# Performance work log

Hardware: AMD Instinct MI355X
Metric: run time of the kernel (lower is better)

The kernel has to match this reference:

```python
import jax, jax.numpy as jnp
import numpy as np

N = 100000      # nodes
F_IN = 500      # num_features
H = 128         # num_hidden
C = 40          # num_classes
E = 3200000     # structural edges
K = 5           # knn neighbors


def setup_inputs() -> dict:
    key = jax.random.key(0)
    ks = jax.random.split(key, 9)
    x = jax.random.normal(ks[0], (N, F_IN), dtype=jnp.float32)
    edge_index = jax.random.randint(ks[1], (2, E), 0, N, dtype=jnp.int64)
    # knn graph: source i repeated K times, targets random (stand-in for cosine-KNN)
    src = jnp.repeat(jnp.arange(N, dtype=jnp.int64), K)
    dst = jax.random.randint(ks[2], (K * N,), 0, N, dtype=jnp.int64)
    edge_index_knn = jnp.stack([src, dst])
    s = lambda f: np.float32(1.0 / np.sqrt(f))
    W1 = jax.random.normal(ks[3], (F_IN, H), jnp.float32) * s(F_IN)
    b1 = jnp.zeros((H,), jnp.float32)
    W2 = jax.random.normal(ks[4], (2 * H, C), jnp.float32) * s(2 * H)
    b2 = jnp.zeros((C,), jnp.float32)
    Wlin = jax.random.normal(ks[5], (C, 2 * C), jnp.float32) * s(2 * C)  # torch Linear layout [out,in]
    blin = jnp.zeros((C,), jnp.float32)
    return {"x": x, "edge_index": edge_index, "edge_index_knn": edge_index_knn,
            "W1": W1, "b1": b1, "W2": W2, "b2": b2, "Wlin": Wlin, "blin": blin}


def gcn_conv(x, W, b, edge_index):
    # PyG GCNConv: add self-loops, symmetric normalization deg^-1/2 A deg^-1/2, x@W, scatter-add, +bias
    n = x.shape[0]
    loop = jnp.arange(n, dtype=edge_index.dtype)
    row = jnp.concatenate([edge_index[0], loop])  # sources (gathered)
    col = jnp.concatenate([edge_index[1], loop])  # targets (scattered)
    deg = jax.ops.segment_sum(jnp.ones_like(col, x.dtype), col, num_segments=n)
    dinv = jnp.where(deg > 0, jax.lax.rsqrt(jnp.maximum(deg, 1e-12)), 0.0).astype(x.dtype)
    norm = dinv[row] * dinv[col]                      # [E+n]
    h = x @ W                                          # [n, out]
    agg = jax.ops.segment_sum(h[row] * norm[:, None], col, num_segments=n)
    return agg + b


def reference(x, edge_index, edge_index_knn, W1, b1, W2, b2, Wlin, blin):
    h1 = gcn_conv(x, W1, b1, edge_index)
    h1_2 = gcn_conv(x, W1, b1, edge_index_knn)
    R1 = jax.nn.relu(jnp.concatenate([h1, h1_2], axis=1))  # dropout identity (eval mode)
    h2 = gcn_conv(R1, W2, b2, edge_index)
    h2_2 = gcn_conv(R1, W2, b2, edge_index_knn)
    R2 = jnp.concatenate([h2, h2_2], axis=1)
    logits = R2 @ Wlin.T + blin
    return jax.nn.log_softmax(logits, axis=1)
```

## Files before the change

kernel.cpp:

```cpp
#include <hip/hip_runtime.h>
#include <stdint.h>

#define NN   100000
#define FIN  500
#define HID  128
#define KP1  512
#define K2   256
#define CO   40
#define NPQ  80
#define NPQP 128
#define NBUCK 391
#define CAPB_S 9216
#define CAPB_K 1536

typedef __attribute__((ext_vector_type(8))) short short8;
typedef __attribute__((ext_vector_type(4))) float float4v;
typedef __attribute__((address_space(3))) unsigned int as3_u32;
typedef __attribute__((address_space(1))) unsigned int as1_u32;

__device__ __forceinline__ unsigned short f2bf(float f) {
  unsigned u = __float_as_uint(f);
  u = u + 0x7fffu + ((u >> 16) & 1u);
  return (unsigned short)(u >> 16);
}
__device__ __forceinline__ float bf2f(unsigned short s) {
  return __uint_as_float(((unsigned)s) << 16);
}
__device__ __forceinline__ void gl_lds16(const void* g, void* l) {
  __builtin_amdgcn_global_load_lds((const as1_u32*)g, (as3_u32*)l, 16, 0, 0);
}

__global__ __launch_bounds__(256) void k_bin(
    const int* __restrict__ ei, int nS, int nb1S, int* __restrict__ gcur_s, int* __restrict__ gbin_s,
    const int* __restrict__ eik, int nK, int* __restrict__ gcur_k, int* __restrict__ gbin_k) {
  __shared__ int cnt[NBUCK];
  __shared__ int base[NBUCK];
  const int b = blockIdx.x;
  const bool knn = (b >= nb1S);
  const int* src = knn ? eik      : ei;
  const int* tgt = knn ? eik + nK : ei + nS;
  const int n    = knn ? nK : nS;
  int* gcur      = knn ? gcur_k : gcur_s;
  int* gbin      = knn ? gbin_k : gbin_s;
  const int capb = knn ? CAPB_K : CAPB_S;
  const int ebase = (knn ? b - nb1S : b) * 4096;
  const int t = threadIdx.x;

  for (int i = t; i < NBUCK; i += 256) cnt[i] = 0;
  __syncthreads();
  int s[16], g[16];
#pragma unroll
  for (int i = 0; i < 16; ++i) {
    const int e = ebase + i * 256 + t;
    const bool v = e < n;
    s[i] = v ? src[e] : 0;
    g[i] = v ? tgt[e] : -1;
    if (v) atomicAdd(&cnt[g[i] >> 8], 1);
  }
  __syncthreads();
  for (int i = t; i < NBUCK; i += 256) {
    const int c = cnt[i];
    base[i] = c ? atomicAdd(&gcur[i], c) : 0;
    cnt[i] = 0;
  }
  __syncthreads();
#pragma unroll
  for (int i = 0; i < 16; ++i) {
    if (g[i] >= 0) {
      const int bkt = g[i] >> 8;
      const int pos = base[bkt] + atomicAdd(&cnt[bkt], 1);
      if (pos < capb) gbin[bkt * capb + pos] = (s[i] << 8) | (g[i] & 255);
    }
  }
}

__global__ __launch_bounds__(512) void k_bscan(const int* __restrict__ gcur_s, int* __restrict__ bscan_s,
                                               const int* __restrict__ gcur_k, int* __restrict__ bscan_k) {
  __shared__ int sd[512];
  const int* gcur = blockIdx.x ? gcur_k : gcur_s;
  int* bscan      = blockIdx.x ? bscan_k : bscan_s;
  const int t = threadIdx.x;
  const int v = (t < NBUCK) ? gcur[t] : 0;
  sd[t] = v;
  __syncthreads();
  for (int off = 1; off < 512; off <<= 1) {
    const int x = (t >= off) ? sd[t - off] : 0;
    __syncthreads(); sd[t] += x; __syncthreads();
  }
  if (t < NBUCK) bscan[t] = sd[t] - v;
}

__global__ __launch_bounds__(256) void k_csr(
    const int* __restrict__ gcur_s, const int* __restrict__ gbin_s, const int* __restrict__ bscan_s,
    int* __restrict__ rp_s, int2* __restrict__ colw_s, float* __restrict__ dinv_s,
    const int* __restrict__ gcur_k, const int* __restrict__ gbin_k, const int* __restrict__ bscan_k,
    int* __restrict__ rp_k, int2* __restrict__ colw_k, float* __restrict__ dinv_k) {
  __shared__ int cnt[256];
  __shared__ int base[256];
  const int b0 = blockIdx.x;
  const bool knn = (b0 >= NBUCK);
  const int b = knn ? b0 - NBUCK : b0;
  const int* gcur  = knn ? gcur_k  : gcur_s;
  const int* gbin  = knn ? gbin_k  : gbin_s;
  const int* bscan = knn ? bscan_k : bscan_s;
  int* rp     = knn ? rp_k   : rp_s;
  int2* colw  = knn ? colw_k : colw_s;
  float* dinv = knn ? dinv_k : dinv_s;
  const int capb = knn ? CAPB_K : CAPB_S;
  const int t = threadIdx.x;
  int nB = gcur[b]; if (nB > capb) nB = capb;
  const int gb0 = b * capb;
  const int gbase = bscan[b];

  cnt[t] = 0;
  __syncthreads();
  for (int i = t; i < nB; i += 256) atomicAdd(&cnt[gbin[gb0 + i] & 255], 1);
  __syncthreads();
  const int myc = cnt[t];
  base[t] = myc;
  __syncthreads();
  for (int off = 1; off < 256; off <<= 1) {
    const int x = (t >= off) ? base[t - off] : 0;
    __syncthreads(); base[t] += x; __syncthreads();
  }
  const int excl = base[t] - myc;
  const int tg = b * 256 + t;
  if (tg < NN) { rp[tg] = gbase + excl; dinv[tg] = rsqrtf((float)(myc + 1)); }
  if (tg == NN) rp[NN] = gbase + excl;
  __syncthreads();
  base[t] = excl; cnt[t] = 0;
  __syncthreads();
  for (int i = t; i < nB; i += 256) {
    const int e = gbin[gb0 + i];
    const int tl = e & 255;
    const int pos = atomicAdd(&cnt[tl], 1);
    colw[gbase + base[tl] + pos] = make_int2(e >> 8, 0);
  }
}

__global__ __launch_bounds__(256) void k_fuse(
    int2* __restrict__ colw_s, const float* __restrict__ dinv_s, int nS, int nbF,
    int2* __restrict__ colw_k, const float* __restrict__ dinv_k, int nK) {
  const int b = blockIdx.x;
  if (b < nbF) {
    const int i = b * 256 + threadIdx.x;
    if (i < nS) {
      const int s = colw_s[i].x;
      colw_s[i].y = __float_as_int(dinv_s[s]);
    }
  } else {
    const int i = (b - nbF) * 256 + threadIdx.x;
    if (i < nK) {
      const int s = colw_k[i].x;
      colw_k[i].y = __float_as_int(dinv_k[s]);
    }
  }
}

__global__ void k_w1t(const float* __restrict__ W1, unsigned short* __restrict__ W1T) {
  int idx = blockIdx.x * 256 + threadIdx.x;
  int n = idx >> 9, k = idx & 511;
  float v = (k < FIN) ? W1[k * HID + n] : 0.f;
  W1T[idx] = f2bf(v);
}
__global__ void k_wpq(const float* __restrict__ W2, const float* __restrict__ Wl,
                      const float* __restrict__ b2, const float* __restrict__ bl,
                      unsigned short* __restrict__ WpqT, float* __restrict__ cb) {
  const int idx = blockIdx.x * 256 + threadIdx.x;
  const int n = idx >> 8, k = idx & 255;
  const int o = (n < CO) ? n : n - CO;
  const int joff = (n < CO) ? 0 : CO;
  float s = 0.f;
#pragma unroll 8
  for (int j = 0; j < CO; ++j) s += W2[k * CO + j] * Wl[o * NPQ + joff + j];
  WpqT[n * K2 + k] = f2bf(s);
  if (blockIdx.x == 0 && threadIdx.x < CO) {
    const int oo = threadIdx.x;
    float c = bl[oo];
    for (int j = 0; j < CO; ++j) c += b2[j] * (Wl[oo * NPQ + j] + Wl[oo * NPQ + CO + j]);
    cb[oo] = c;
  }
}

__global__ __launch_bounds__(256) void k_gemm1(const float* __restrict__ x,
    const unsigned short* __restrict__ W1T, const float* __restrict__ zbuf,
    unsigned short* __restrict__ H1b) {
  __shared__ float Als[2][512 * 4];
  __shared__ unsigned short Bls[2][512 * 8];
  const int t = threadIdx.x;
  const int wv = t >> 6, lane = t & 63;
  const int qd = lane >> 4, mr = lane & 15;
  const int m0 = blockIdx.x * 64;

  float4v acc[8];
  const float4v zf4 = {0.f, 0.f, 0.f, 0.f};
#pragma unroll
  for (int b = 0; b < 8; ++b) acc[b] = zf4;

  auto stage = [&](int kk, int pb) {
    const int k0 = kk * 32;
#pragma unroll
    for (int i = 0; i < 2; ++i) {
      const int q = (wv * 2 + i) * 64 + lane;
      const int m = q >> 3;
      const int kg = (q & 7) ^ (m & 7);
      const int gm = m0 + m, kb = k0 + kg * 4;
      const float* gp = (gm < NN && kb < FIN) ? (x + (size_t)gm * FIN + kb) : zbuf;
      gl_lds16(gp, &Als[pb][q * 4]);
    }
#pragma unroll
    for (int i = 0; i < 2; ++i) {
      const int q = (wv * 2 + i) * 64 + lane;
      const int n = q >> 2;
      const int kg = (q & 3) ^ ((q >> 3) & 3);
      gl_lds16(W1T + n * KP1 + k0 + kg * 8, &Bls[pb][q * 8]);
    }
  };

  stage(0, 0);
  for (int kk = 0; kk < 16; ++kk) {
    const int cur = kk & 1;
    if (kk + 1 < 16) {
      stage(kk + 1, cur ^ 1);
      asm volatile("s_waitcnt vmcnt(4)" ::: "memory");
    } else {
      asm volatile("s_waitcnt vmcnt(0)" ::: "memory");
    }
    __builtin_amdgcn_s_barrier();

    short8 af;
    {
      const int m = wv * 16 + mr;
      const int s0 = m * 8 + ((2 * qd) ^ (m & 7));
      const int s1 = m * 8 + ((2 * qd + 1) ^ (m & 7));
      const float4v a0 = *(const float4v*)&Als[cur][s0 * 4];
      const float4v a1 = *(const float4v*)&Als[cur][s1 * 4];
      af[0] = (short)f2bf(a0[0]); af[1] = (short)f2bf(a0[1]);
      af[2] = (short)f2bf(a0[2]); af[3] = (short)f2bf(a0[3]);
      af[4] = (short)f2bf(a1[0]); af[5] = (short)f2bf(a1[1]);
      af[6] = (short)f2bf(a1[2]); af[7] = (short)f2bf(a1[3]);
    }
#pragma unroll
    for (int ct = 0; ct < 8; ++ct) {
      const int n = ct * 16 + mr;
      const int sb = n * 4 + (qd ^ ((n >> 1) & 3));
      const short8 bf = *(const short8*)&Bls[cur][sb * 8];
      acc[ct] = __builtin_amdgcn_mfma_f32_16x16x32_bf16(af, bf, acc[ct], 0, 0, 0);
    }
    __builtin_amdgcn_s_barrier();
  }

  const int rb = m0 + wv * 16 + qd * 4;
#pragma unroll
  for (int ct = 0; ct < 8; ++ct) {
    const int col = ct * 16 + mr;
#pragma unroll
    for (int j = 0; j < 4; ++j) {
      const int r = rb + j;
      if (r < NN) H1b[(size_t)r * HID + col] = f2bf(acc[ct][j]);
    }
  }
}

__global__ __launch_bounds__(256) void k_gemm2(const unsigned short* __restrict__ R1b,
    const unsigned short* __restrict__ WpqT, const unsigned short* __restrict__ zbuf,
    unsigned short* __restrict__ PQ) {
  __shared__ unsigned short Als[2][256 * 8];
  __shared__ unsigned short Bls[2][512 * 8];
  const int t = threadIdx.x;
  const int wv = t >> 6, lane = t & 63;
  const int qd = lane >> 4, mr = lane & 15;
  const int m0 = blockIdx.x * 64;

  float4v acc[5];
  const float4v zf4 = {0.f, 0.f, 0.f, 0.f};
#pragma unroll
  for (int b = 0; b < 5; ++b) acc[b] = zf4;

  auto stage = [&](int kk, int pb) {
    const int k0 = kk * 32;
    {
      const int q = wv * 64 + lane;
      const int m = q >> 2;
      const int kg = (q & 3) ^ ((q >> 3) & 3);
      const int gm = m0 + m;
      const unsigned short* gp = (gm < NN) ? (R1b + (size_t)gm * K2 + k0 + kg * 8) : zbuf;
      gl_lds16(gp, &Als[pb][q * 8]);
    }
#pragma unroll
    for (int i = 0; i < 2; ++i) {
      const int q = (wv * 2 + i) * 64 + lane;
      const int n = q >> 2;
      const int kg = (q & 3) ^ ((q >> 3) & 3);
      gl_lds16(WpqT + n * K2 + k0 + kg * 8, &Bls[pb][q * 8]);
    }
  };

  stage(0, 0);
  for (int kk = 0; kk < 8; ++kk) {
    const int cur = kk & 1;
    if (kk + 1 < 8) {
      stage(kk + 1, cur ^ 1);
      asm volatile("s_waitcnt vmcnt(3)" ::: "memory");
    } else {
      asm volatile("s_waitcnt vmcnt(0)" ::: "memory");
    }
    __builtin_amdgcn_s_barrier();

    short8 af;
    {
      const int m = wv * 16 + mr;
      const int sa = m * 4 + (qd ^ ((m >> 1) & 3));
      af = *(const short8*)&Als[cur][sa * 8];
    }
#pragma unroll
    for (int ct = 0; ct < 5; ++ct) {
      const int n = ct * 16 + mr;
      const int sb = n * 4 + (qd ^ ((n >> 1) & 3));
      const short8 bf = *(const short8*)&Bls[cur][sb * 8];
      acc[ct] = __builtin_amdgcn_mfma_f32_16x16x32_bf16(af, bf, acc[ct], 0, 0, 0);
    }
    __builtin_amdgcn_s_barrier();
  }

  const int rb = m0 + wv * 16 + qd * 4;
#pragma unroll
  for (int ct = 0; ct < 5; ++ct) {
    const int col = ct * 16 + mr;
#pragma unroll
    for (int j = 0; j < 4; ++j) {
      const int r = rb + j;
      if (r < NN) PQ[(size_t)r * NPQ + col] = f2bf(acc[ct][j]);
    }
  }
}

__device__ __forceinline__ void ld8(const int2* __restrict__ cw, int base, int e1, bool full,
                                    int2* __restrict__ q) {
  if (full) {
#pragma unroll
    for (int j = 0; j < 8; ++j) q[j] = cw[base + j];
  } else {
    const int e1c = e1 - 1;
#pragma unroll
    for (int j = 0; j < 8; ++j) {
      const int ee = base + j;
      int2 t = cw[(ee < e1) ? ee : e1c];
      t.y = (ee < e1) ? t.y : 0;
      q[j] = t;
    }
  }
}
__device__ __forceinline__ void g8(const int2* __restrict__ q,
    const unsigned* __restrict__ H32, int lane, unsigned* __restrict__ d) {
#pragma unroll
  for (int j = 0; j < 8; ++j) d[j] = H32[(size_t)q[j].x * 64 + lane];
}
__device__ __forceinline__ void f8(const int2* __restrict__ q, const unsigned* __restrict__ d,
                                   float& ax, float& ay) {
#pragma unroll
  for (int j = 0; j < 8; ++j) {
    const float w = __int_as_float(q[j].y);
    ax += w * __uint_as_float(d[j] << 16);
    ay += w * __uint_as_float(d[j] & 0xffff0000u);
  }
}

__global__ __launch_bounds__(256) void k_agg1(
    const int* __restrict__ rp_s, const int2* __restrict__ colw_s, const float* __restrict__ dinv_s,
    const int* __restrict__ rp_k, const int2* __restrict__ colw_k, const float* __restrict__ dinv_k,
    const unsigned short* __restrict__ H, const float* __restrict__ bias,
    unsigned short* __restrict__ out) {
  const int wv = threadIdx.x >> 6, lane = threadIdx.x & 63;
  const int c = blockIdx.x * 4 + wv;
  if (c >= NN) return;
  const unsigned* H32 = (const unsigned*)H;
  const int e0s = __builtin_amdgcn_readfirstlane(rp_s[c]);
  const int e1s = __builtin_amdgcn_readfirstlane(rp_s[c + 1]);
  const int e0k = __builtin_amdgcn_readfirstlane(rp_k[c]);
  const int e1k = __builtin_amdgcn_readfirstlane(rp_k[c + 1]);
  const int nbS = (e1s - e0s + 7) >> 3;
  const int nbK = (e1k - e0k + 7) >> 3;

  int2 q0[8], q1[8], qk[8];
  unsigned d0[8], d1[8], dk[8];
  const unsigned pc = H32[(size_t)c * 64 + lane];
  if (nbS > 0) { ld8(colw_s, e0s, e1s, e0s + 8 <= e1s, q0); g8(q0, H32, lane, d0); }
  if (nbS > 1) { ld8(colw_s, e0s + 8, e1s, e0s + 16 <= e1s, q1); g8(q1, H32, lane, d1); }
  if (nbK > 0) { ld8(colw_k, e0k, e1k, e0k + 8 <= e1k, qk); g8(qk, H32, lane, dk); }

  const float dcs = dinv_s[c], dck = dinv_k[c];
  const float slo = __uint_as_float(pc << 16);
  const float shi = __uint_as_float(pc & 0xffff0000u);
  float ax = dcs * slo, ay = dcs * shi;
  float bx = dck * slo, by = dck * shi;

  int b = 0;
  while (b + 2 < nbS) {
    f8(q0, d0, ax, ay);
    {
      const int bs = e0s + (b + 2) * 8;
      ld8(colw_s, bs, e1s, bs + 8 <= e1s, q0);
      g8(q0, H32, lane, d0);
    }
    f8(q1, d1, ax, ay);
    if (b + 3 < nbS) {
      const int bs = e0s + (b + 3) * 8;
      ld8(colw_s, bs, e1s, bs + 8 <= e1s, q1);
      g8(q1, H32, lane, d1);
    }
    b += 2;
  }
  if (b < nbS) f8(q0, d0, ax, ay);
  if (b + 1 < nbS) f8(q1, d1, ax, ay);

  if (nbK > 0) f8(qk, dk, bx, by);
  for (int bk = 1; bk < nbK; ++bk) {
    const int bs = e0k + bk * 8;
    ld8(colw_k, bs, e1k, bs + 8 <= e1k, qk);
    g8(qk, H32, lane, dk);
    f8(qk, dk, bx, by);
  }

  const float2 bb = ((const float2*)bias)[lane];
  const float o0 = fmaxf(dcs * ax + bb.x, 0.f);
  const float o1 = fmaxf(dcs * ay + bb.y, 0.f);
  const float o2 = fmaxf(dck * bx + bb.x, 0.f);
  const float o3 = fmaxf(dck * by + bb.y, 0.f);
  unsigned* orow = (unsigned*)(out + (size_t)c * K2);
  orow[lane]      = (unsigned)f2bf(o0) | ((unsigned)f2bf(o1) << 16);
  orow[64 + lane] = (unsigned)f2bf(o2) | ((unsigned)f2bf(o3) << 16);
}

__global__ __launch_bounds__(256) void k_aggf(
    const int* __restrict__ rp_s, const int2* __restrict__ colw_s, const float* __restrict__ dinv_s,
    const int* __restrict__ rp_k, const int2* __restrict__ colw_k, const float* __restrict__ dinv_k,
    const unsigned short* __restrict__ PQ, const float* __restrict__ cb,
    float* __restrict__ out) {
  const int wv = threadIdx.x >> 6, lane = threadIdx.x & 63;
  const int c = blockIdx.x * 4 + wv;
  if (c >= NN) return;
  const unsigned* PQ32 = (const unsigned*)PQ;
  const int g = lane / 20;
  const int l = lane % 20;
  float sx = 0.f, sy = 0.f, kx = 0.f, ky = 0.f;
  if (g < 3) {
    {
      const int e1 = rp_s[c + 1];
      int e = rp_s[c] + g;
      for (; e + 9 < e1; e += 12) {
        const int2 q0 = colw_s[e], q1 = colw_s[e + 3], q2 = colw_s[e + 6], q3 = colw_s[e + 9];
        const unsigned d0 = PQ32[(size_t)q0.x * 40 + l];
        const unsigned d1 = PQ32[(size_t)q1.x * 40 + l];
        const unsigned d2 = PQ32[(size_t)q2.x * 40 + l];
        const unsigned d3 = PQ32[(size_t)q3.x * 40 + l];
        const float w0 = __int_as_float(q0.y), w1 = __int_as_float(q1.y);
        const float w2 = __int_as_float(q2.y), w3 = __int_as_float(q3.y);
        sx += w0 * __uint_as_float(d0 << 16) + w1 * __uint_as_float(d1 << 16)
            + w2 * __uint_as_float(d2 << 16) + w3 * __uint_as_float(d3 << 16);
        sy += w0 * __uint_as_float(d0 & 0xffff0000u) + w1 * __uint_as_float(d1 & 0xffff0000u)
            + w2 * __uint_as_float(d2 & 0xffff0000u) + w3 * __uint_as_float(d3 & 0xffff0000u);
      }
      for (; e < e1; e += 3) {
        const int2 q = colw_s[e];
        const unsigned d = PQ32[(size_t)q.x * 40 + l];
        const float w = __int_as_float(q.y);
        sx += w * __uint_as_float(d << 16);
        sy += w * __uint_as_float(d & 0xffff0000u);
      }
    }
    {
      const int e1 = rp_k[c + 1];
      int e = rp_k[c] + g;
      for (; e < e1; e += 3) {
        const int2 q = colw_k[e];
        const unsigned d = PQ32[(size_t)q.x * 40 + 20 + l];
        const float w = __int_as_float(q.y);
        kx += w * __uint_as_float(d << 16);
        ky += w * __uint_as_float(d & 0xffff0000u);
      }
    }
  }
  sx += __shfl(sx, lane + 20) + __shfl(sx, lane + 40);
  sy += __shfl(sy, lane + 20) + __shfl(sy, lane + 40);
  kx += __shfl(kx, lane + 20) + __shfl(kx, lane + 40);
  ky += __shfl(ky, lane + 20) + __shfl(ky, lane + 40);

  float lo = 0.f, hi = 0.f;
  if (lane < 20) {
    const float dcs = dinv_s[c], dck = dinv_k[c];
    const unsigned dP = PQ32[(size_t)c * 40 + lane];
    const unsigned dQ = PQ32[(size_t)c * 40 + 20 + lane];
    const float2 cbb = ((const float2*)cb)[lane];
    lo = dcs * (sx + dcs * __uint_as_float(dP << 16))
       + dck * (kx + dck * __uint_as_float(dQ << 16)) + cbb.x;
    hi = dcs * (sy + dcs * __uint_as_float(dP & 0xffff0000u))
       + dck * (ky + dck * __uint_as_float(dQ & 0xffff0000u)) + cbb.y;
  }
  float m = (lane < 20) ? fmaxf(lo, hi) : -3.4e38f;
#pragma unroll
  for (int off = 1; off < 64; off <<= 1) m = fmaxf(m, __shfl_xor(m, off));
  float s = (lane < 20) ? (expf(lo - m) + expf(hi - m)) : 0.f;
#pragma unroll
  for (int off = 1; off < 64; off <<= 1) s += __shfl_xor(s, off);
  const float lse = m + logf(s);
  if (lane < 20) {
    float2 o; o.x = lo - lse; o.y = hi - lse;
    ((float2*)(out + (size_t)c * CO))[lane] = o;
  }
}

extern "C" void kernel_launch(void* const* d_in, const int* in_sizes, int n_in,
                              void* d_out, int out_size, void* d_ws, size_t ws_size,
                              hipStream_t stream) {
  const float* x  = (const float*)d_in[0];
  const int* ei   = (const int*)d_in[1];
  const int* eik  = (const int*)d_in[2];
  const float* W1 = (const float*)d_in[3];
  const float* b1 = (const float*)d_in[4];
  const float* W2 = (const float*)d_in[5];
  const float* b2 = (const float*)d_in[6];
  const float* Wl = (const float*)d_in[7];
  const float* bl = (const float*)d_in[8];
  float* out = (float*)d_out;
  const int E  = in_sizes[1] / 2;
  const int EK = in_sizes[2] / 2;

  char* p = (char*)d_ws;
  size_t off = 0;
  auto alloc = [&](size_t bytes) -> void* {
    void* r = (void*)(p + off);
    off += (bytes + 255) & ~(size_t)255;
    return r;
  };
  int* gcur_s = (int*)alloc((size_t)NBUCK * 4);
  int* gcur_k = (int*)alloc((size_t)NBUCK * 4);
  void* zbuf = alloc(256);
  const size_t zero_span = off;
  int* bscan_s = (int*)alloc((size_t)NBUCK * 4);
  int* bscan_k = (int*)alloc((size_t)NBUCK * 4);
  float* dinv_s = (float*)alloc((size_t)NN * 4);
  float* dinv_k = (float*)alloc((size_t)NN * 4);
  int* rp_s = (int*)alloc((size_t)(NN + 1) * 4);
  int* rp_k = (int*)alloc((size_t)(NN + 1) * 4);
  unsigned short* W1T = (unsigned short*)alloc((size_t)HID * KP1 * 2);
  unsigned short* WpqT = (unsigned short*)alloc((size_t)NPQP * K2 * 2);
  float* cbv = (float*)alloc((size_t)CO * 4);
  int* gbin_s = (int*)alloc((size_t)NBUCK * CAPB_S * 4);
  int* gbin_k = (int*)alloc((size_t)NBUCK * CAPB_K * 4);
  int2* colw_s = (int2*)alloc((size_t)E * 8);
  int2* colw_k = (int2*)alloc((size_t)EK * 8);
  unsigned short* H1b = (unsigned short*)alloc((size_t)NN * HID * 2);
  unsigned short* R1b = (unsigned short*)alloc((size_t)NN * K2 * 2);
  unsigned short* PQ = H1b;

  hipMemsetAsync(d_ws, 0, zero_span, stream);

  const int nb1S = (E + 4095) / 4096;
  const int nb1K = (EK + 4095) / 4096;
  k_bin<<<nb1S + nb1K, 256, 0, stream>>>(ei, E, nb1S, gcur_s, gbin_s, eik, EK, gcur_k, gbin_k);
  k_bscan<<<2, 512, 0, stream>>>(gcur_s, bscan_s, gcur_k, bscan_k);
  k_csr<<<2 * NBUCK, 256, 0, stream>>>(gcur_s, gbin_s, bscan_s, rp_s, colw_s, dinv_s,
                                       gcur_k, gbin_k, bscan_k, rp_k, colw_k, dinv_k);
  const int nbF = (E + 255) / 256;
  const int nbFk = (EK + 255) / 256;
  k_fuse<<<nbF + nbFk, 256, 0, stream>>>(colw_s, dinv_s, E, nbF, colw_k, dinv_k, EK);

  k_w1t<<<(HID * KP1) / 256, 256, 0, stream>>>(W1, W1T);
  k_wpq<<<NPQ, 256, 0, stream>>>(W2, Wl, b2, bl, WpqT, cbv);

  k_gemm1<<<(NN + 63) / 64, 256, 0, stream>>>(x, W1T, (const float*)zbuf, H1b);
  const int nbAgg = (NN + 3) / 4;
  k_agg1<<<nbAgg, 256, 0, stream>>>(rp_s, colw_s, dinv_s, rp_k, colw_k, dinv_k, H1b, b1, R1b);

  k_gemm2<<<(NN + 63) / 64, 256, 0, stream>>>(R1b, WpqT, (const unsigned short*)zbuf, PQ);
  k_aggf<<<nbAgg, 256, 0, stream>>>(rp_s, colw_s, dinv_s, rp_k, colw_k, dinv_k, PQ, cbv, out);
}
```

Measured before the change: 688.8 us.

## Software-pipeline edge-block gathers in final aggregation kernel with double buffering

Rewrites k_aggf so each wave loads 12-edge blocks of CSR entries with wave-uniform bounds taken through readfirstlane. The PQ gathers for the next two structural blocks are issued before the current block is accumulated, so gather latency overlaps with the FMAs. Partial blocks are padded by clamping the index and zeroing the weight, and the self-row PQ loads are hoisted to the start of the kernel. The cost is higher register pressure from three 12-entry buffers, plus redundant gathers on padded and idle lanes.

Measured after the change: 671.8 us. -2.5%, faster.

```diff
diff --git a/kernel.cpp b/kernel.cpp
--- a/kernel.cpp
+++ b/kernel.cpp
@@ -432,6 +432,43 @@
   orow[64 + lane] = (unsigned)f2bf(o2) | ((unsigned)f2bf(o3) << 16);
 }
 
+__device__ __forceinline__ void ld12(const int2* __restrict__ cw, int base, int e1, bool full,
+                                     int2* __restrict__ q) {
+  if (full) {
+#pragma unroll
+    for (int j = 0; j < 12; ++j) q[j] = cw[base + j];
+  } else {
+    const int e1c = e1 - 1;
+#pragma unroll
+    for (int j = 0; j < 12; ++j) {
+      const int ee = base + j;
+      int2 t = cw[(ee < e1) ? ee : e1c];
+      t.y = (ee < e1) ? t.y : 0;
+      q[j] = t;
+    }
+  }
+}
+__device__ __forceinline__ void gt4(const int2* __restrict__ q, const unsigned* __restrict__ PQ32,
+                                    int g, int l, int off, float* __restrict__ w,
+                                    unsigned* __restrict__ d) {
+#pragma unroll
+  for (int t = 0; t < 4; ++t) {
+    const int2 qa = q[3 * t], qb = q[3 * t + 1], qc = q[3 * t + 2];
+    const int xs = (g == 0) ? qa.x : ((g == 1) ? qb.x : qc.x);
+    const int wi = (g == 0) ? qa.y : ((g == 1) ? qb.y : qc.y);
+    w[t] = __int_as_float(wi);
+    d[t] = PQ32[(size_t)xs * 40 + off + l];
+  }
+}
+__device__ __forceinline__ void ct4(const float* __restrict__ w, const unsigned* __restrict__ d,
+                                    float& sx, float& sy) {
+#pragma unroll
+  for (int t = 0; t < 4; ++t) {
+    sx += w[t] * __uint_as_float(d[t] << 16);
+    sy += w[t] * __uint_as_float(d[t] & 0xffff0000u);
+  }
+}
+
 __global__ __launch_bounds__(256) void k_aggf(
     const int* __restrict__ rp_s, const int2* __restrict__ colw_s, const float* __restrict__ dinv_s,
     const int* __restrict__ rp_k, const int2* __restrict__ colw_k, const float* __restrict__ dinv_k,
@@ -441,46 +478,57 @@
   const int c = blockIdx.x * 4 + wv;
   if (c >= NN) return;
   const unsigned* PQ32 = (const unsigned*)PQ;
-  const int g = lane / 20;
-  const int l = lane % 20;
+  const int g = (lane < 60) ? (lane / 20) : 2;
+  const int l = lane - 20 * g;
+
+  const int e0s = __builtin_amdgcn_readfirstlane(rp_s[c]);
+  const int e1s = __builtin_amdgcn_readfirstlane(rp_s[c + 1]);
+  const int e0k = __builtin_amdgcn_readfirstlane(rp_k[c]);
+  const int e1k = __builtin_amdgcn_readfirstlane(rp_k[c + 1]);
+  const int nbS = (e1s - e0s + 11) / 12;
+  const int nbK = (e1k - e0k + 11) / 12;
+
+  unsigned dP = 0, dQ = 0;
+  if (lane < 20) {
+    dP = PQ32[(size_t)c * 40 + lane];
+    dQ = PQ32[(size_t)c * 40 + 20 + lane];
+  }
+
+  int2 q0[12], q1[12], qk[12];
+  float w0[4], w1[4], wk[4];
+  unsigned d0[4], d1[4], dk[4];
+  if (nbS > 0) { ld12(colw_s, e0s, e1s, e0s + 12 <= e1s, q0); gt4(q0, PQ32, g, l, 0, w0, d0); }
+  if (nbS > 1) { ld12(colw_s, e0s + 12, e1s, e0s + 24 <= e1s, q1); gt4(q1, PQ32, g, l, 0, w1, d1); }
+  if (nbK > 0) { ld12(colw_k, e0k, e1k, e0k + 12 <= e1k, qk); gt4(qk, PQ32, g, l, 20, wk, dk); }
+
   float sx = 0.f, sy = 0.f, kx = 0.f, ky = 0.f;
-  if (g < 3) {
+  int b = 0;
+  while (b + 2 < nbS) {
+    ct4(w0, d0, sx, sy);
     {
-      const int e1 = rp_s[c + 1];
-      int e = rp_s[c] + g;
-      for (; e + 9 < e1; e += 12) {
-        const int2 q0 = colw_s[e], q1 = colw_s[e + 3], q2 = colw_s[e + 6], q3 = colw_s[e + 9];
-        const unsigned d0 = PQ32[(size_t)q0.x * 40 + l];
-        const unsigned d1 = PQ32[(size_t)q1.x * 40 + l];
-        const unsigned d2 = PQ32[(size_t)q2.x * 40 + l];
-        const unsigned d3 = PQ32[(size_t)q3.x * 40 + l];
-        const float w0 = __int_as_float(q0.y), w1 = __int_as_float(q1.y);
-        const float w2 = __int_as_float(q2.y), w3 = __int_as_float(q3.y);
-        sx += w0 * __uint_as_float(d0 << 16) + w1 * __uint_as_float(d1 << 16)
-            + w2 * __uint_as_float(d2 << 16) + w3 * __uint_as_float(d3 << 16);
-        sy += w0 * __uint_as_float(d0 & 0xffff0000u) + w1 * __uint_as_float(d1 & 0xffff0000u)
-            + w2 * __uint_as_float(d2 & 0xffff0000u) + w3 * __uint_as_float(d3 & 0xffff0000u);
-      }
-      for (; e < e1; e += 3) {
-        const int2 q = colw_s[e];
-        const unsigned d = PQ32[(size_t)q.x * 40 + l];
-        const float w = __int_as_float(q.y);
-        sx += w * __uint_as_float(d << 16);
-        sy += w * __uint_as_float(d & 0xffff0000u);
-      }
-    }
-    {
-      const int e1 = rp_k[c + 1];
-      int e = rp_k[c] + g;
-      for (; e < e1; e += 3) {
-        const int2 q = colw_k[e];
-        const unsigned d = PQ32[(size_t)q.x * 40 + 20 + l];
-        const float w = __int_as_float(q.y);
-        kx += w * __uint_as_float(d << 16);
-        ky += w * __uint_as_float(d & 0xffff0000u);
-      }
-    }
-  }
+      const int bs = e0s + (b + 2) * 12;
+      ld12(colw_s, bs, e1s, bs + 12 <= e1s, q0);
+      gt4(q0, PQ32, g, l, 0, w0, d0);
+    }
+    ct4(w1, d1, sx, sy);
+    if (b + 3 < nbS) {
+      const int bs = e0s + (b + 3) * 12;
+      ld12(colw_s, bs, e1s, bs + 12 <= e1s, q1);
+      gt4(q1, PQ32, g, l, 0, w1, d1);
+    }
+    b += 2;
+  }
+  if (b < nbS) ct4(w0, d0, sx, sy);
+  if (b + 1 < nbS) ct4(w1, d1, sx, sy);
+
+  if (nbK > 0) ct4(wk, dk, kx, ky);
+  for (int bk = 1; bk < nbK; ++bk) {
+    const int bs = e0k + bk * 12;
+    ld12(colw_k, bs, e1k, bs + 12 <= e1k, qk);
+    gt4(qk, PQ32, g, l, 20, wk, dk);
+    ct4(wk, dk, kx, ky);
+  }
+
   sx += __shfl(sx, lane + 20) + __shfl(sx, lane + 40);
   sy += __shfl(sy, lane + 20) + __shfl(sy, lane + 40);
   kx += __shfl(kx, lane + 20) + __shfl(kx, lane + 40);
@@ -489,8 +537,6 @@
   float lo = 0.f, hi = 0.f;
   if (lane < 20) {
     const float dcs = dinv_s[c], dck = dinv_k[c];
-    const unsigned dP = PQ32[(size_t)c * 40 + lane];
-    const unsigned dQ = PQ32[(size_t)c * 40 + 20 + lane];
     const float2 cbb = ((const float2*)cb)[lane];
     lo = dcs * (sx + dcs * __uint_as_float(dP << 16))
        + dck * (kx + dck * __uint_as_float(dQ << 16)) + cbb.x;
```
